# Kernel tuning notes

Measured on AMD Instinct MI355X. Metric: run time of the kernel, lower is better.

## Reference

```python
import jax, jax.numpy as jnp
import numpy as np
from jax import lax

DIM = 384
NUM_HEADS = 6
STRIDE_Q = 1
STRIDE_KV = 2
BN_EPS = 1e-5
SCALE = DIM ** (-0.5)  # CvT scales by dim_out, not head_dim


def setup_inputs() -> dict:
    key = jax.random.key(0)
    ks = jax.random.split(key, 8)
    B, H, W, C = 32, 28, 28, DIM
    T = 1 + H * W
    x = jax.random.normal(ks[0], (B, T, C), dtype=jnp.float32)
    conv_w = jax.random.normal(ks[1], (3, C, 1, 3, 3), dtype=jnp.float32) * 0.1
    bn_gamma = jnp.ones((3, C), dtype=jnp.float32)
    bn_beta = jnp.zeros((3, C), dtype=jnp.float32)
    bn_mean = jnp.zeros((3, C), dtype=jnp.float32)
    bn_var = jnp.ones((3, C), dtype=jnp.float32)
    w_q = jax.random.normal(ks[2], (C, C), dtype=jnp.float32) * 0.02
    w_k = jax.random.normal(ks[3], (C, C), dtype=jnp.float32) * 0.02
    w_v = jax.random.normal(ks[4], (C, C), dtype=jnp.float32) * 0.02
    w_proj = jax.random.normal(ks[5], (C, C), dtype=jnp.float32) * 0.02
    b_proj = jnp.zeros((C,), dtype=jnp.float32)
    return {"x": x, "conv_w": conv_w, "bn_gamma": bn_gamma, "bn_beta": bn_beta,
            "bn_mean": bn_mean, "bn_var": bn_var, "w_q": w_q, "w_k": w_k,
            "w_v": w_v, "w_proj": w_proj, "b_proj": b_proj, "h": H, "w": W}


def _dw_conv_bn(x_sp, cw, gamma, beta, mean, var, stride):
    # x_sp: [B, C, H, W]; cw: [C, 1, 3, 3] depthwise (groups=C); inference BN
    C = x_sp.shape[1]
    y = lax.conv_general_dilated(
        x_sp, cw, window_strides=(stride, stride), padding=((1, 1), (1, 1)),
        feature_group_count=C, dimension_numbers=("NCHW", "OIHW", "NCHW"))
    inv = gamma * lax.rsqrt(var + BN_EPS)
    y = y * inv[None, :, None, None] + (beta - mean * inv)[None, :, None, None]
    B, Cc, Hc, Wc = y.shape
    return y.reshape(B, Cc, Hc * Wc).transpose(0, 2, 1)  # b (h w) c


def reference(x, conv_w, bn_gamma, bn_beta, bn_mean, bn_var,
              w_q, w_k, w_v, w_proj, b_proj, h, w):
    B, T, C = x.shape
    nh, hd = NUM_HEADS, C // NUM_HEADS
    cls_tok, x_tok = x[:, :1], x[:, 1:]
    x_sp = x_tok.reshape(B, h, w, C).transpose(0, 3, 1, 2)  # b c h w

    q = _dw_conv_bn(x_sp, conv_w[0], bn_gamma[0], bn_beta[0], bn_mean[0], bn_var[0], STRIDE_Q)
    k = _dw_conv_bn(x_sp, conv_w[1], bn_gamma[1], bn_beta[1], bn_mean[1], bn_var[1], STRIDE_KV)
    v = _dw_conv_bn(x_sp, conv_w[2], bn_gamma[2], bn_beta[2], bn_mean[2], bn_var[2], STRIDE_KV)

    q = jnp.concatenate([cls_tok, q], axis=1)
    k = jnp.concatenate([cls_tok, k], axis=1)
    v = jnp.concatenate([cls_tok, v], axis=1)

    def split_heads(t, wm):  # linear proj then b t (h d) -> b h t d
        t = t @ wm.T
        Bt, Tt, _ = t.shape
        return t.reshape(Bt, Tt, nh, hd).transpose(0, 2, 1, 3)

    q = split_heads(q, w_q)
    k = split_heads(k, w_k)
    v = split_heads(v, w_v)

    attn = jax.nn.softmax(jnp.einsum("bhld,bhtd->bhlt", q, k) * SCALE, axis=-1)
    out = jnp.einsum("bhlt,bhtd->bhld", attn, v)
    out = out.transpose(0, 2, 1, 3).reshape(B, -1, C)  # b t (h d)
    return out @ w_proj.T + b_proj
```

## Files before the change

kernel.cpp:

```cpp
#include <hip/hip_runtime.h>
#include <math.h>

#define B_SZ   32
#define C_DIM  384
#define H_IN   28
#define W_IN   28
#define TQ     785
#define TKV    197
#define NH     6
#define HD     64
#define SCALE_F 0.05103103630798287f
#define SCALE_L2E (0.05103103630798287f * 1.4426950408889634f)
#define BN_EPS_F 1e-5f

#define QROWS    25120
#define KVROWS   6304
#define QROWS_P  25344
#define KVROWS_P 6400
#define WELEM    147456
#define VT_LD    208

#define QT256    99
#define KVT256   25

typedef _Float16 f16;
typedef f16  f16x8 __attribute__((ext_vector_type(8)));
typedef f16  f16x4 __attribute__((ext_vector_type(4)));
typedef float f32x4 __attribute__((ext_vector_type(4)));

__device__ __forceinline__ void split16(float v, f16& h, f16& l) {
    h = (f16)v;
    l = (f16)(v - (float)h);
}

__device__ __forceinline__ void cp16(void* lds, const void* g) {
    __builtin_amdgcn_global_load_lds(
        (const __attribute__((address_space(1))) unsigned int*)g,
        (__attribute__((address_space(3))) unsigned int*)lds, 16, 0, 0);
}

__device__ __forceinline__ bool swz(int id, int yMax, int& y, int& n0) {
    int g = id / 24, w = id - g * 24;
    y = g * 8 + (w & 7);
    n0 = (w >> 3) * 128;
    return y < yMax;
}

__global__ __launch_bounds__(256) void prep_kernel(
    const float* __restrict__ wq, const float* __restrict__ wk,
    const float* __restrict__ wv, const float* __restrict__ wp,
    const float* __restrict__ conv_w,
    const float* __restrict__ gamma, const float* __restrict__ beta,
    const float* __restrict__ mean, const float* __restrict__ var,
    f16* __restrict__ Wh, f16* __restrict__ Wl,
    float* __restrict__ wAll)
{
    int idx = blockIdx.x * 256 + threadIdx.x;
    if (idx < 4 * WELEM) {
        int which = idx / WELEM, rem = idx - which * WELEM;
        const float* s = (which == 0) ? wq : (which == 1) ? wk : (which == 2) ? wv : wp;
        float v = s[rem];
        if (which == 0) v *= SCALE_L2E;
        f16 h, l;
        split16(v, h, l);
        Wh[idx] = h; Wl[idx] = l;
    } else if (idx < 4 * WELEM + 3 * C_DIM) {
        int k = idx - 4 * WELEM;
        int cv = k / C_DIM, c = k - cv * C_DIM;
        float inv = gamma[k] * rsqrtf(var[k] + BN_EPS_F);
#pragma unroll
        for (int t = 0; t < 9; ++t)
            wAll[cv * 3840 + t * C_DIM + c] = conv_w[(size_t)cv * C_DIM * 9 + c * 9 + t] * inv;
        wAll[cv * 3840 + 9 * C_DIM + c] = beta[k] - mean[k] * inv;
    }
}

__global__ __launch_bounds__(256) void fused_conv_kernel(
    const float* __restrict__ x,
    const float* __restrict__ wAll,
    f16* __restrict__ qh, f16* __restrict__ ql,
    f16* __restrict__ kh, f16* __restrict__ kl,
    f16* __restrict__ vh, f16* __restrict__ vl)
{
    __shared__ float sW[3 * 3840];
    int tid = threadIdx.x;
    int oi = blockIdx.x, b = blockIdx.y;

    if (oi == H_IN) {
        if (tid < 96) {
            int c = tid * 4;
            float4 v = *(const float4*)&x[(size_t)b * TQ * C_DIM + c];
            float a[4] = {v.x, v.y, v.z, v.w};
            f16x4 hv, lv;
#pragma unroll
            for (int u = 0; u < 4; ++u) { f16 h, l; split16(a[u], h, l); hv[u] = h; lv[u] = l; }
            size_t oq = (size_t)b * TQ * C_DIM + c;
            size_t okv = (size_t)b * TKV * C_DIM + c;
            *(f16x4*)&qh[oq] = hv;  *(f16x4*)&ql[oq] = lv;
            *(f16x4*)&kh[okv] = hv; *(f16x4*)&kl[okv] = lv;
            *(f16x4*)&vh[okv] = hv; *(f16x4*)&vl[okv] = lv;
        }
        return;
    }

#pragma unroll
    for (int i = 0; i < 12; ++i) {
        int idx = tid + 256 * i;
        if (idx < 2880) cp16(&sW[idx * 4], &wAll[idx * 4]);
    }
    __syncthreads();

    const size_t xb = (size_t)b * TQ * C_DIM + C_DIM;
    bool oi_even = (oi & 1) == 0;

    for (int it = 0; it < 11; ++it) {
        int idx = tid + 256 * it;
        if (idx >= 28 * 96) break;
        int oj = idx / 96, cg = idx - oj * 96;
        int c = cg * 4;

        float4 xv[9];
#pragma unroll
        for (int di = 0; di < 3; ++di) {
            int ii = oi + di - 1;
            bool rok = (ii >= 0) && (ii < H_IN);
#pragma unroll
            for (int dj = 0; dj < 3; ++dj) {
                int jj = oj + dj - 1;
                bool ok = rok && (jj >= 0) && (jj < W_IN);
                xv[di * 3 + dj] = ok ? *(const float4*)&x[xb + ((size_t)ii * W_IN + jj) * C_DIM + c]
                                     : make_float4(0.f, 0.f, 0.f, 0.f);
            }
        }

        {
            float4 acc = *(const float4*)&sW[0 * 3840 + 9 * C_DIM + c];
#pragma unroll
            for (int t = 0; t < 9; ++t) {
                float4 w4 = *(const float4*)&sW[0 * 3840 + t * C_DIM + c];
                acc.x += w4.x * xv[t].x; acc.y += w4.y * xv[t].y;
                acc.z += w4.z * xv[t].z; acc.w += w4.w * xv[t].w;
            }
            f16x4 hv, lv;
            float a[4] = {acc.x, acc.y, acc.z, acc.w};
#pragma unroll
            for (int u = 0; u < 4; ++u) { f16 h, l; split16(a[u], h, l); hv[u] = h; lv[u] = l; }
            size_t off = ((size_t)b * TQ + 1 + oi * W_IN + oj) * C_DIM + c;
            *(f16x4*)&qh[off] = hv;
            *(f16x4*)&ql[off] = lv;
        }

        if (oi_even && ((oj & 1) == 0)) {
            int p = (oi >> 1) * 14 + (oj >> 1);
            size_t off = ((size_t)b * TKV + 1 + p) * C_DIM + c;
#pragma unroll
            for (int cv = 1; cv <= 2; ++cv) {
                float4 acc = *(const float4*)&sW[cv * 3840 + 9 * C_DIM + c];
#pragma unroll
                for (int t = 0; t < 9; ++t) {
                    float4 w4 = *(const float4*)&sW[cv * 3840 + t * C_DIM + c];
                    acc.x += w4.x * xv[t].x; acc.y += w4.y * xv[t].y;
                    acc.z += w4.z * xv[t].z; acc.w += w4.w * xv[t].w;
                }
                f16x4 hv, lv;
                float a[4] = {acc.x, acc.y, acc.z, acc.w};
#pragma unroll
                for (int u = 0; u < 4; ++u) { f16 h, l; split16(a[u], h, l); hv[u] = h; lv[u] = l; }
                if (cv == 1) { *(f16x4*)&kh[off] = hv; *(f16x4*)&kl[off] = lv; }
                else         { *(f16x4*)&vh[off] = hv; *(f16x4*)&vl[off] = lv; }
            }
        }
    }
}

__device__ __forceinline__ void gemm_body(
    const f16* __restrict__ Ah, const f16* __restrict__ Al,
    const f16* __restrict__ Wh, const f16* __restrict__ Wl,
    const float* __restrict__ bias,
    float* __restrict__ Cf, f16* __restrict__ Coh, f16* __restrict__ Col,
    int M, int mode, int m0, int n0)
{
    __shared__ f16 lds[3 * 24576];

    const int t = threadIdx.x;
    const int wv = t >> 6, lane = t & 63;
    const int wr = (wv >> 1) * 64;
    const int wc = (wv & 1) * 64;
    const int lrow = lane & 15, quad = lane >> 4;
    const int qsw = quad ^ ((lrow >> 1) & 3);

    const int sr = t >> 2;
    const int g  = (t & 3) ^ ((t >> 3) & 3);

    const f16* gA0h = Ah + (size_t)(m0 + sr) * 384 + g * 8;
    const f16* gA1h = gA0h + 128 * 384;
    const f16* gA0l = Al + (size_t)(m0 + sr) * 384 + g * 8;
    const f16* gA1l = gA0l + 128 * 384;
    const f16* gBh  = Wh + (size_t)(n0 + sr) * 384 + g * 8;
    const f16* gBl  = Wl + (size_t)(n0 + sr) * 384 + g * 8;

#define STAGE(buf, kk) do {                                   \
        f16* d = lds + (buf) * 24576 + t * 8;                 \
        const int ko = (kk) * 32;                             \
        cp16(d,         gA0h + ko);                           \
        cp16(d + 4096,  gA1h + ko);                           \
        cp16(d + 8192,  gA0l + ko);                           \
        cp16(d + 12288, gA1l + ko);                           \
        cp16(d + 16384, gBh + ko);                            \
        cp16(d + 20480, gBl + ko);                            \
    } while (0)

    f32x4 acc[4][4];
#pragma unroll
    for (int i = 0; i < 4; ++i)
#pragma unroll
        for (int j = 0; j < 4; ++j)
            acc[i][j] = (f32x4){0.f, 0.f, 0.f, 0.f};

    STAGE(0, 0);
    STAGE(1, 1);

#pragma unroll
    for (int kk = 0; kk < 12; ++kk) {
        if (kk == 11) asm volatile("s_waitcnt vmcnt(0)" ::: "memory");
        else          asm volatile("s_waitcnt vmcnt(6)" ::: "memory");
        __builtin_amdgcn_s_barrier();
        __builtin_amdgcn_sched_barrier(0);

        if (kk < 10) {
            STAGE((kk + 2) % 3, kk + 2);
            __builtin_amdgcn_sched_barrier(0);
        }

        const f16* bp = lds + (kk % 3) * 24576;
        f16x8 ah[4], al[4], bh[4], bl[4];
#pragma unroll
        for (int i = 0; i < 4; ++i) {
            int ro = (wr + i * 16 + lrow) * 32 + qsw * 8;
            ah[i] = *(const f16x8*)&bp[ro];
            al[i] = *(const f16x8*)&bp[8192 + ro];
        }
#pragma unroll
        for (int j = 0; j < 4; ++j) {
            int ro = (wc + j * 16 + lrow) * 32 + qsw * 8;
            bh[j] = *(const f16x8*)&bp[16384 + ro];
            bl[j] = *(const f16x8*)&bp[20480 + ro];
        }
        asm volatile("s_waitcnt lgkmcnt(0)" ::: "memory");
        __builtin_amdgcn_sched_barrier(0);

        __builtin_amdgcn_s_setprio(1);
#pragma unroll
        for (int i = 0; i < 4; ++i)
#pragma unroll
            for (int j = 0; j < 4; ++j) {
                acc[i][j] = __builtin_amdgcn_mfma_f32_16x16x32_f16(ah[i], bh[j], acc[i][j], 0, 0, 0);
                acc[i][j] = __builtin_amdgcn_mfma_f32_16x16x32_f16(ah[i], bl[j], acc[i][j], 0, 0, 0);
                acc[i][j] = __builtin_amdgcn_mfma_f32_16x16x32_f16(al[i], bh[j], acc[i][j], 0, 0, 0);
            }
        __builtin_amdgcn_s_setprio(0);
    }
#undef STAGE

#pragma unroll
    for (int i = 0; i < 4; ++i) {
        int grow0 = m0 + wr + i * 16 + quad * 4;
#pragma unroll
        for (int j = 0; j < 4; ++j) {
            int gcol = n0 + wc + j * 16 + lrow;
            float bb = (bias && mode == 0) ? bias[gcol] : 0.f;
#pragma unroll
            for (int r = 0; r < 4; ++r) {
                int grow = grow0 + r;
                if (grow >= M) continue;
                float v = acc[i][j][r] + bb;
                if (mode == 0) {
                    Cf[(size_t)grow * 384 + gcol] = v;
                } else if (mode == 1) {
                    f16 h, l;
                    split16(v, h, l);
                    Coh[(size_t)grow * 384 + gcol] = h;
                    Col[(size_t)grow * 384 + gcol] = l;
                } else {
                    int bb2 = grow / TKV;
                    int key = grow - bb2 * TKV;
                    size_t off = (size_t)bb2 * 384 * VT_LD + (size_t)gcol * VT_LD + key;
                    f16 h, l;
                    split16(v, h, l);
                    Coh[off] = h;
                    Col[off] = l;
                }
            }
        }
    }
}

__global__ __launch_bounds__(512, 2) void qkv_proj_kernel(
    const f16* __restrict__ qh, const f16* __restrict__ ql,
    const f16* __restrict__ kh, const f16* __restrict__ kl,
    const f16* __restrict__ vh, const f16* __restrict__ vl,
    const f16* __restrict__ Wh, const f16* __restrict__ Wl,
    f16* __restrict__ Qph, f16* __restrict__ Qpl,
    f16* __restrict__ Kph, f16* __restrict__ Kpl,
    f16* __restrict__ VTh, f16* __restrict__ VTl,
    int yMax)
{
    int y, n0;
    if (!swz(blockIdx.x, yMax, y, n0)) return;
    if (y < QT256)
        gemm_body(qh, ql, Wh, Wl, nullptr, nullptr, Qph, Qpl, QROWS, 1, y * 256, n0);
    else if (y < QT256 + KVT256)
        gemm_body(kh, kl, Wh + WELEM, Wl + WELEM, nullptr, nullptr, Kph, Kpl,
                  KVROWS, 1, (y - QT256) * 256, n0);
    else
        gemm_body(vh, vl, Wh + 2 * WELEM, Wl + 2 * WELEM, nullptr, nullptr, VTh, VTl,
                  KVROWS, 2, (y - QT256 - KVT256) * 256, n0);
}

__global__ __launch_bounds__(512, 2) void v_proj_kernel(
    const f16* __restrict__ vh, const f16* __restrict__ vl,
    const f16* __restrict__ Wh, const f16* __restrict__ Wl,
    f16* __restrict__ VTh, f16* __restrict__ VTl)
{
    int y, n0;
    if (!swz(blockIdx.x, KVT256, y, n0)) return;
    gemm_body(vh, vl, Wh, Wl, nullptr, nullptr, VTh, VTl, KVROWS, 2, y * 256, n0);
}

__global__ __launch_bounds__(512, 2) void out_proj_kernel(
    const f16* __restrict__ Ah, const f16* __restrict__ Al,
    const f16* __restrict__ Wh, const f16* __restrict__ Wl,
    const float* __restrict__ bias, float* __restrict__ Cf)
{
    int y, n0;
    if (!swz(blockIdx.x, QT256, y, n0)) return;
    gemm_body(Ah, Al, Wh, Wl, bias, Cf, nullptr, nullptr, QROWS, 0, y * 256, n0);
}

__global__ __launch_bounds__(256) void attn_mfma4(
    const f16* __restrict__ Qh, const f16* __restrict__ Ql,
    const f16* __restrict__ Kh, const f16* __restrict__ Kl,
    const f16* __restrict__ VTh, const f16* __restrict__ VTl,
    f16* __restrict__ Oh, f16* __restrict__ Ol)
{
    __shared__ f16 sQh[2][64][32];
    __shared__ f16 sQl[2][64][32];
    __shared__ f16 sKh[2][64][32];
    __shared__ f16 sKl[2][64][32];
    __shared__ float sPs[64][68];

    int t = threadIdx.x;
    int wv = t >> 6, lane = t & 63;
    int c = lane & 15, quad = lane >> 4;
    int wq0 = wv * 16;
    int h = blockIdx.y, b = blockIdx.z;
    int q0 = blockIdx.x * 64;

    const size_t qbase  = (size_t)b * TQ * C_DIM + h * HD;
    const size_t kbase  = (size_t)b * TKV * C_DIM + h * HD;
    const size_t vtbase = (size_t)b * 384 * VT_LD + (size_t)h * HD * VT_LD;

#pragma unroll
    for (int i = 0; i < 2; ++i) {
        int idx = t + 256 * i;
        int ks = idx >> 8, row = (idx >> 2) & 63, sg = (idx & 3) * 8;
        cp16(&sQh[ks][row][sg], &Qh[qbase + (size_t)(q0 + row) * C_DIM + ks * 32 + sg]);
        cp16(&sQl[ks][row][sg], &Ql[qbase + (size_t)(q0 + row) * C_DIM + ks * 32 + sg]);
    }

    f32x4 s[4][4];
#pragma unroll
    for (int kt = 0; kt < 4; ++kt)
#pragma unroll
        for (int j = 0; j < 4; ++j)
            s[kt][j] = (f32x4){0.f, 0.f, 0.f, 0.f};

#pragma unroll
    for (int kt = 0; kt < 4; ++kt) {
        if (kt) __syncthreads();
#pragma unroll
        for (int i = 0; i < 2; ++i) {
            int idx = t + 256 * i;
            int ks = idx >> 8, row = (idx >> 2) & 63, sg = (idx & 3) * 8;
            cp16(&sKh[ks][row][sg], &Kh[kbase + (size_t)(kt * 64 + row) * C_DIM + ks * 32 + sg]);
            cp16(&sKl[ks][row][sg], &Kl[kbase + (size_t)(kt * 64 + row) * C_DIM + ks * 32 + sg]);
        }
        __syncthreads();

#pragma unroll
        for (int ks = 0; ks < 2; ++ks) {
            f16x8 qh8 = *(const f16x8*)&sQh[ks][wq0 + c][quad * 8];
            f16x8 ql8 = *(const f16x8*)&sQl[ks][wq0 + c][quad * 8];
#pragma unroll
            for (int j = 0; j < 4; ++j) {
                f16x8 kh8 = *(const f16x8*)&sKh[ks][j * 16 + c][quad * 8];
                f16x8 kl8 = *(const f16x8*)&sKl[ks][j * 16 + c][quad * 8];
                s[kt][j] = __builtin_amdgcn_mfma_f32_16x16x32_f16(qh8, kh8, s[kt][j], 0, 0, 0);
                s[kt][j] = __builtin_amdgcn_mfma_f32_16x16x32_f16(qh8, kl8, s[kt][j], 0, 0, 0);
                s[kt][j] = __builtin_amdgcn_mfma_f32_16x16x32_f16(ql8, kh8, s[kt][j], 0, 0, 0);
            }
        }
    }

    __syncthreads();

#pragma unroll
    for (int i = 0; i < 2; ++i) {
        int idx = t + 256 * i;
        int ks = idx >> 8, row = (idx >> 2) & 63, sg = (idx & 3) * 8;
        cp16(&sKh[ks][row][sg], &VTh[vtbase + (size_t)row * VT_LD + ks * 32 + sg]);
        cp16(&sKl[ks][row][sg], &VTl[vtbase + (size_t)row * VT_LD + ks * 32 + sg]);
    }

#pragma unroll
    for (int r = 0; r < 4; ++r) {
        s[3][0][r] = (c < 5) ? s[3][0][r] : -1e30f;
        s[3][1][r] = -1e30f;
        s[3][2][r] = -1e30f;
        s[3][3][r] = -1e30f;
    }

    float inv_r[4];
#pragma unroll
    for (int r = 0; r < 4; ++r) {
        float mx = -1e30f;
#pragma unroll
        for (int kt = 0; kt < 4; ++kt)
#pragma unroll
            for (int j = 0; j < 4; ++j)
                mx = fmaxf(mx, s[kt][j][r]);
        mx = fmaxf(mx, __shfl_xor(mx, 1));
        mx = fmaxf(mx, __shfl_xor(mx, 2));
        mx = fmaxf(mx, __shfl_xor(mx, 4));
        mx = fmaxf(mx, __shfl_xor(mx, 8));
        float sum = 0.f;
#pragma unroll
        for (int kt = 0; kt < 4; ++kt)
#pragma unroll
            for (int j = 0; j < 4; ++j) {
                float pv = exp2f(s[kt][j][r] - mx);
                s[kt][j][r] = pv;
                sum += pv;
            }
        sum += __shfl_xor(sum, 1);
        sum += __shfl_xor(sum, 2);
        sum += __shfl_xor(sum, 4);
        sum += __shfl_xor(sum, 8);
        inv_r[r] = 1.f / sum;
    }

    f32x4 o[4];
#pragma unroll
    for (int j = 0; j < 4; ++j) o[j] = (f32x4){0.f, 0.f, 0.f, 0.f};

#pragma unroll
    for (int vt = 0; vt < 4; ++vt) {
#pragma unroll
        for (int r = 0; r < 4; ++r)
#pragma unroll
            for (int j = 0; j < 4; ++j)
                sPs[wq0 + quad * 4 + r][j * 16 + c] = s[vt][j][r];

        __syncthreads();

#pragma unroll
        for (int ks = 0; ks < 2; ++ks) {
            float4 p0 = *(const float4*)&sPs[wq0 + c][ks * 32 + quad * 8];
            float4 p1 = *(const float4*)&sPs[wq0 + c][ks * 32 + quad * 8 + 4];
            float pf[8] = {p0.x, p0.y, p0.z, p0.w, p1.x, p1.y, p1.z, p1.w};
            f16x8 ph8, pl8;
#pragma unroll
            for (int ii = 0; ii < 8; ++ii) {
                f16 hh, ll;
                split16(pf[ii], hh, ll);
                ph8[ii] = hh; pl8[ii] = ll;
            }
#pragma unroll
            for (int j = 0; j < 4; ++j) {
                f16x8 vh8 = *(const f16x8*)&sKh[ks][j * 16 + c][quad * 8];
                f16x8 vl8 = *(const f16x8*)&sKl[ks][j * 16 + c][quad * 8];
                o[j] = __builtin_amdgcn_mfma_f32_16x16x32_f16(ph8, vh8, o[j], 0, 0, 0);
                o[j] = __builtin_amdgcn_mfma_f32_16x16x32_f16(ph8, vl8, o[j], 0, 0, 0);
                o[j] = __builtin_amdgcn_mfma_f32_16x16x32_f16(pl8, vh8, o[j], 0, 0, 0);
            }
        }

        if (vt < 3) {
            __syncthreads();
#pragma unroll
            for (int i = 0; i < 2; ++i) {
                int idx = t + 256 * i;
                int ks = idx >> 8, row = (idx >> 2) & 63, sg = (idx & 3) * 8;
                cp16(&sKh[ks][row][sg],
                     &VTh[vtbase + (size_t)row * VT_LD + (vt + 1) * 64 + ks * 32 + sg]);
                cp16(&sKl[ks][row][sg],
                     &VTl[vtbase + (size_t)row * VT_LD + (vt + 1) * 64 + ks * 32 + sg]);
            }
        }
    }

#pragma unroll
    for (int r = 0; r < 4; ++r) {
        int gq = q0 + wq0 + quad * 4 + r;
        if (gq >= TQ) continue;
        float inv = inv_r[r];
#pragma unroll
        for (int j = 0; j < 4; ++j) {
            float v = o[j][r] * inv;
            f16 hh, ll;
            split16(v, hh, ll);
            size_t off = (size_t)(b * TQ + gq) * C_DIM + h * HD + j * 16 + c;
            Oh[off] = hh;
            Ol[off] = ll;
        }
    }
}

extern "C" void kernel_launch(void* const* d_in, const int* in_sizes, int n_in,
                              void* d_out, int out_size, void* d_ws, size_t ws_size,
                              hipStream_t stream) {
    const float* x       = (const float*)d_in[0];
    const float* conv_w  = (const float*)d_in[1];
    const float* bn_g    = (const float*)d_in[2];
    const float* bn_b    = (const float*)d_in[3];
    const float* bn_m    = (const float*)d_in[4];
    const float* bn_v    = (const float*)d_in[5];
    const float* w_q     = (const float*)d_in[6];
    const float* w_k     = (const float*)d_in[7];
    const float* w_v     = (const float*)d_in[8];
    const float* w_proj  = (const float*)d_in[9];
    const float* b_proj  = (const float*)d_in[10];
    float* out = (float*)d_out;

    const size_t QSZ   = (size_t)QROWS_P * 384 * sizeof(f16);
    const size_t KVSZ  = (size_t)KVROWS_P * 384 * sizeof(f16);
    const size_t WSZ   = 4 * (size_t)WELEM * sizeof(f16);
    const size_t VTSZ  = (size_t)B_SZ * 384 * VT_LD * sizeof(f16);
    const size_t WALLS = 3 * 3840 * sizeof(float);

    char* p = (char*)d_ws;
    f16* qh  = (f16*)p; p += QSZ;
    f16* ql  = (f16*)p; p += QSZ;
    f16* vh  = (f16*)p; p += KVSZ;
    f16* vl  = (f16*)p; p += KVSZ;
    f16* kh  = (f16*)p; p += KVSZ;
    f16* kl  = (f16*)p; p += KVSZ;
    f16* Wh  = (f16*)p; p += WSZ;
    f16* Wl  = (f16*)p; p += WSZ;
    f16* Qph = (f16*)p; p += QSZ;
    f16* Qpl = (f16*)p; p += QSZ;
    f16* Kph = (f16*)p; p += KVSZ;
    f16* Kpl = (f16*)p; p += KVSZ;
    float* wAll = (float*)p; p += WALLS;

    size_t used = (size_t)(p - (char*)d_ws);
    bool sepVT = (ws_size >= used + 2 * VTSZ);
    f16 *VTh, *VTl;
    if (sepVT) {
        VTh = (f16*)p;
        VTl = VTh + (size_t)B_SZ * 384 * VT_LD;
    } else {
        VTh = kh;
        VTl = VTh + (size_t)B_SZ * 384 * VT_LD;
    }
    f16* oh = qh;
    f16* ol = ql;

    {
        int total = 4 * WELEM + 3 * C_DIM;
        prep_kernel<<<(total + 255) / 256, 256, 0, stream>>>(
            w_q, w_k, w_v, w_proj, conv_w, bn_g, bn_b, bn_m, bn_v, Wh, Wl, wAll);
    }

    {
        dim3 gc(H_IN + 1, B_SZ);
        fused_conv_kernel<<<gc, 256, 0, stream>>>(x, wAll, qh, ql, kh, kl, vh, vl);
    }

    if (sepVT) {
        int yMax = QT256 + 2 * KVT256;
        int nb = ((yMax + 7) / 8) * 24;
        qkv_proj_kernel<<<nb, 512, 0, stream>>>(qh, ql, kh, kl, vh, vl, Wh, Wl,
                                                Qph, Qpl, Kph, Kpl, VTh, VTl, yMax);
    } else {
        int yMax = QT256 + KVT256;
        int nb = ((yMax + 7) / 8) * 24;
        qkv_proj_kernel<<<nb, 512, 0, stream>>>(qh, ql, kh, kl, vh, vl, Wh, Wl,
                                                Qph, Qpl, Kph, Kpl, VTh, VTl, yMax);
        int nbv = ((KVT256 + 7) / 8) * 24;
        v_proj_kernel<<<nbv, 512, 0, stream>>>(vh, vl, Wh + 2 * WELEM, Wl + 2 * WELEM,
                                               VTh, VTl);
    }

    {
        dim3 ga((TQ + 63) / 64, NH, B_SZ);
        attn_mfma4<<<ga, 256, 0, stream>>>(Qph, Qpl, Kph, Kpl, VTh, VTl, oh, ol);
    }

    {
        int nb = ((QT256 + 7) / 8) * 24;
        out_proj_kernel<<<nb, 512, 0, stream>>>(oh, ol, Wh + 3 * WELEM, Wl + 3 * WELEM,
                                                b_proj, out);
    }
}
```

Before: 303.3 us.

## Drop low-half split for V, attention probs and attention output

Stores V^T, the softmax probabilities and the attention output as single fp16 instead of hi/lo split pairs. This cuts the PV MFMAs from three per tile to one and removes the Vl/Ol buffers. The output projection gets a new lighter GEMM body that loads only the A high part, uses a three-stage LDS pipeline and issues two MFMAs per tile. The V tile prefetch is rescheduled into double buffers across the four key tiles. In exchange, accuracy for V, P and O drops to plain fp16.

After: 271.6 us. 1.12x faster.

```diff
diff --git a/kernel.cpp b/kernel.cpp
--- a/kernel.cpp
+++ b/kernel.cpp
@@ -16,7 +16,7 @@
 #define QROWS    25120
 #define KVROWS   6304
 #define QROWS_P  25344
-#define KVROWS_P 6400
+#define KVROWS_P 6528
 #define WELEM    147456
 #define VT_LD    208
 
@@ -285,11 +285,107 @@
                     int bb2 = grow / TKV;
                     int key = grow - bb2 * TKV;
                     size_t off = (size_t)bb2 * 384 * VT_LD + (size_t)gcol * VT_LD + key;
-                    f16 h, l;
-                    split16(v, h, l);
-                    Coh[off] = h;
-                    Col[off] = l;
+                    Coh[off] = (f16)v;
                 }
+            }
+        }
+    }
+}
+
+__device__ __forceinline__ void gemm_body_s(
+    const f16* __restrict__ Ah,
+    const f16* __restrict__ Wh, const f16* __restrict__ Wl,
+    const float* __restrict__ bias, float* __restrict__ Cf,
+    int M, int m0, int n0)
+{
+    __shared__ f16 lds[3 * 16384];
+
+    const int t = threadIdx.x;
+    const int wv = t >> 6, lane = t & 63;
+    const int wr = (wv >> 1) * 64;
+    const int wc = (wv & 1) * 64;
+    const int lrow = lane & 15, quad = lane >> 4;
+    const int qsw = quad ^ ((lrow >> 1) & 3);
+
+    const int sr = t >> 2;
+    const int g  = (t & 3) ^ ((t >> 3) & 3);
+
+    const f16* gA0 = Ah + (size_t)(m0 + sr) * 384 + g * 8;
+    const f16* gA1 = gA0 + 128 * 384;
+    const f16* gBh = Wh + (size_t)(n0 + sr) * 384 + g * 8;
+    const f16* gBl = Wl + (size_t)(n0 + sr) * 384 + g * 8;
+
+#define STAGE_S(buf, kk) do {                                 \
+        f16* d = lds + (buf) * 16384 + t * 8;                 \
+        const int ko = (kk) * 32;                             \
+        cp16(d,         gA0 + ko);                            \
+        cp16(d + 4096,  gA1 + ko);                            \
+        cp16(d + 8192,  gBh + ko);                            \
+        cp16(d + 12288, gBl + ko);                            \
+    } while (0)
+
+    f32x4 acc[4][4];
+#pragma unroll
+    for (int i = 0; i < 4; ++i)
+#pragma unroll
+        for (int j = 0; j < 4; ++j)
+            acc[i][j] = (f32x4){0.f, 0.f, 0.f, 0.f};
+
+    STAGE_S(0, 0);
+    STAGE_S(1, 1);
+
+#pragma unroll
+    for (int kk = 0; kk < 12; ++kk) {
+        if (kk == 11) asm volatile("s_waitcnt vmcnt(0)" ::: "memory");
+        else          asm volatile("s_waitcnt vmcnt(4)" ::: "memory");
+        __builtin_amdgcn_s_barrier();
+        __builtin_amdgcn_sched_barrier(0);
+
+        if (kk < 10) {
+            STAGE_S((kk + 2) % 3, kk + 2);
+            __builtin_amdgcn_sched_barrier(0);
+        }
+
+        const f16* bp = lds + (kk % 3) * 16384;
+        f16x8 ah[4], bh[4], bl[4];
+#pragma unroll
+        for (int i = 0; i < 4; ++i) {
+            int ro = (wr + i * 16 + lrow) * 32 + qsw * 8;
+            ah[i] = *(const f16x8*)&bp[ro];
+        }
+#pragma unroll
+        for (int j = 0; j < 4; ++j) {
+            int ro = (wc + j * 16 + lrow) * 32 + qsw * 8;
+            bh[j] = *(const f16x8*)&bp[8192 + ro];
+            bl[j] = *(const f16x8*)&bp[12288 + ro];
+        }
+        asm volatile("s_waitcnt lgkmcnt(0)" ::: "memory");
+        __builtin_amdgcn_sched_barrier(0);
+
+        __builtin_amdgcn_s_setprio(1);
+#pragma unroll
+        for (int i = 0; i < 4; ++i)
+#pragma unroll
+            for (int j = 0; j < 4; ++j) {
+                acc[i][j] = __builtin_amdgcn_mfma_f32_16x16x32_f16(ah[i], bh[j], acc[i][j], 0, 0, 0);
+                acc[i][j] = __builtin_amdgcn_mfma_f32_16x16x32_f16(ah[i], bl[j], acc[i][j], 0, 0, 0);
+            }
+        __builtin_amdgcn_s_setprio(0);
+    }
+#undef STAGE_S
+
+#pragma unroll
+    for (int i = 0; i < 4; ++i) {
+        int grow0 = m0 + wr + i * 16 + quad * 4;
+#pragma unroll
+        for (int j = 0; j < 4; ++j) {
+            int gcol = n0 + wc + j * 16 + lrow;
+            float bb = bias[gcol];
+#pragma unroll
+            for (int r = 0; r < 4; ++r) {
+                int grow = grow0 + r;
+                if (grow >= M) continue;
+                Cf[(size_t)grow * 384 + gcol] = acc[i][j][r] + bb;
             }
         }
     }
@@ -302,7 +398,7 @@
     const f16* __restrict__ Wh, const f16* __restrict__ Wl,
     f16* __restrict__ Qph, f16* __restrict__ Qpl,
     f16* __restrict__ Kph, f16* __restrict__ Kpl,
-    f16* __restrict__ VTh, f16* __restrict__ VTl,
+    f16* __restrict__ VTh,
     int yMax)
 {
     int y, n0;
@@ -313,35 +409,35 @@
         gemm_body(kh, kl, Wh + WELEM, Wl + WELEM, nullptr, nullptr, Kph, Kpl,
                   KVROWS, 1, (y - QT256) * 256, n0);
     else
-        gemm_body(vh, vl, Wh + 2 * WELEM, Wl + 2 * WELEM, nullptr, nullptr, VTh, VTl,
+        gemm_body(vh, vl, Wh + 2 * WELEM, Wl + 2 * WELEM, nullptr, nullptr, VTh, nullptr,
                   KVROWS, 2, (y - QT256 - KVT256) * 256, n0);
 }
 
 __global__ __launch_bounds__(512, 2) void v_proj_kernel(
     const f16* __restrict__ vh, const f16* __restrict__ vl,
     const f16* __restrict__ Wh, const f16* __restrict__ Wl,
-    f16* __restrict__ VTh, f16* __restrict__ VTl)
+    f16* __restrict__ VTh)
 {
     int y, n0;
     if (!swz(blockIdx.x, KVT256, y, n0)) return;
-    gemm_body(vh, vl, Wh, Wl, nullptr, nullptr, VTh, VTl, KVROWS, 2, y * 256, n0);
+    gemm_body(vh, vl, Wh, Wl, nullptr, nullptr, VTh, nullptr, KVROWS, 2, y * 256, n0);
 }
 
 __global__ __launch_bounds__(512, 2) void out_proj_kernel(
-    const f16* __restrict__ Ah, const f16* __restrict__ Al,
+    const f16* __restrict__ Ah,
     const f16* __restrict__ Wh, const f16* __restrict__ Wl,
     const float* __restrict__ bias, float* __restrict__ Cf)
 {
     int y, n0;
     if (!swz(blockIdx.x, QT256, y, n0)) return;
-    gemm_body(Ah, Al, Wh, Wl, bias, Cf, nullptr, nullptr, QROWS, 0, y * 256, n0);
-}
-
-__global__ __launch_bounds__(256) void attn_mfma4(
+    gemm_body_s(Ah, Wh, Wl, bias, Cf, QROWS, y * 256, n0);
+}
+
+__global__ __launch_bounds__(256) void attn_mfma6(
     const f16* __restrict__ Qh, const f16* __restrict__ Ql,
     const f16* __restrict__ Kh, const f16* __restrict__ Kl,
-    const f16* __restrict__ VTh, const f16* __restrict__ VTl,
-    f16* __restrict__ Oh, f16* __restrict__ Ol)
+    const f16* __restrict__ VTh,
+    f16* __restrict__ Oh)
 {
     __shared__ f16 sQh[2][64][32];
     __shared__ f16 sQl[2][64][32];
@@ -409,7 +505,7 @@
         int idx = t + 256 * i;
         int ks = idx >> 8, row = (idx >> 2) & 63, sg = (idx & 3) * 8;
         cp16(&sKh[ks][row][sg], &VTh[vtbase + (size_t)row * VT_LD + ks * 32 + sg]);
-        cp16(&sKl[ks][row][sg], &VTl[vtbase + (size_t)row * VT_LD + ks * 32 + sg]);
+        cp16(&sKl[ks][row][sg], &VTh[vtbase + (size_t)row * VT_LD + 64 + ks * 32 + sg]);
     }
 
 #pragma unroll
@@ -453,51 +549,46 @@
 #pragma unroll
     for (int j = 0; j < 4; ++j) o[j] = (f32x4){0.f, 0.f, 0.f, 0.f};
 
-#pragma unroll
-    for (int vt = 0; vt < 4; ++vt) {
-#pragma unroll
-        for (int r = 0; r < 4; ++r)
-#pragma unroll
-            for (int j = 0; j < 4; ++j)
-                sPs[wq0 + quad * 4 + r][j * 16 + c] = s[vt][j][r];
-
-        __syncthreads();
-
-#pragma unroll
-        for (int ks = 0; ks < 2; ++ks) {
-            float4 p0 = *(const float4*)&sPs[wq0 + c][ks * 32 + quad * 8];
-            float4 p1 = *(const float4*)&sPs[wq0 + c][ks * 32 + quad * 8 + 4];
-            float pf[8] = {p0.x, p0.y, p0.z, p0.w, p1.x, p1.y, p1.z, p1.w};
-            f16x8 ph8, pl8;
-#pragma unroll
-            for (int ii = 0; ii < 8; ++ii) {
-                f16 hh, ll;
-                split16(pf[ii], hh, ll);
-                ph8[ii] = hh; pl8[ii] = ll;
-            }
-#pragma unroll
-            for (int j = 0; j < 4; ++j) {
-                f16x8 vh8 = *(const f16x8*)&sKh[ks][j * 16 + c][quad * 8];
-                f16x8 vl8 = *(const f16x8*)&sKl[ks][j * 16 + c][quad * 8];
-                o[j] = __builtin_amdgcn_mfma_f32_16x16x32_f16(ph8, vh8, o[j], 0, 0, 0);
-                o[j] = __builtin_amdgcn_mfma_f32_16x16x32_f16(ph8, vl8, o[j], 0, 0, 0);
-                o[j] = __builtin_amdgcn_mfma_f32_16x16x32_f16(pl8, vh8, o[j], 0, 0, 0);
-            }
-        }
-
-        if (vt < 3) {
-            __syncthreads();
-#pragma unroll
-            for (int i = 0; i < 2; ++i) {
-                int idx = t + 256 * i;
-                int ks = idx >> 8, row = (idx >> 2) & 63, sg = (idx & 3) * 8;
-                cp16(&sKh[ks][row][sg],
-                     &VTh[vtbase + (size_t)row * VT_LD + (vt + 1) * 64 + ks * 32 + sg]);
-                cp16(&sKl[ks][row][sg],
-                     &VTl[vtbase + (size_t)row * VT_LD + (vt + 1) * 64 + ks * 32 + sg]);
-            }
-        }
-    }
+#define SPS_WRITE(VT) do {                                           \
+        _Pragma("unroll") for (int r = 0; r < 4; ++r)                \
+            _Pragma("unroll") for (int j = 0; j < 4; ++j)            \
+                sPs[wq0 + quad * 4 + r][j * 16 + c] = s[VT][j][r];   \
+    } while (0)
+
+#define VT_ISSUE2(DST, VT) do {                                                \
+        _Pragma("unroll") for (int i = 0; i < 2; ++i) {                        \
+            int idx = t + 256 * i;                                             \
+            int ks = idx >> 8, row = (idx >> 2) & 63, sg = (idx & 3) * 8;      \
+            cp16(&DST[ks][row][sg],                                            \
+                 &VTh[vtbase + (size_t)row * VT_LD + (VT) * 64 + ks * 32 + sg]); \
+        } } while (0)
+
+#define PV_TILE_S(BUF) do {                                                    \
+        _Pragma("unroll") for (int ks = 0; ks < 2; ++ks) {                     \
+            float4 p0 = *(const float4*)&sPs[wq0 + c][ks * 32 + quad * 8];     \
+            float4 p1 = *(const float4*)&sPs[wq0 + c][ks * 32 + quad * 8 + 4]; \
+            float pf[8] = {p0.x, p0.y, p0.z, p0.w, p1.x, p1.y, p1.z, p1.w};    \
+            f16x8 p8;                                                          \
+            _Pragma("unroll") for (int ii = 0; ii < 8; ++ii) p8[ii] = (f16)pf[ii]; \
+            _Pragma("unroll") for (int j = 0; j < 4; ++j) {                    \
+                f16x8 vv8 = *(const f16x8*)&BUF[ks][j * 16 + c][quad * 8];     \
+                o[j] = __builtin_amdgcn_mfma_f32_16x16x32_f16(p8, vv8, o[j], 0, 0, 0); \
+            } } } while (0)
+
+    __syncthreads();
+    SPS_WRITE(0);
+    PV_TILE_S(sKh);
+    __syncthreads();
+    VT_ISSUE2(sKh, 2);
+    SPS_WRITE(1);
+    PV_TILE_S(sKl);
+    __syncthreads();
+    VT_ISSUE2(sKl, 3);
+    SPS_WRITE(2);
+    PV_TILE_S(sKh);
+    __syncthreads();
+    SPS_WRITE(3);
+    PV_TILE_S(sKl);
 
 #pragma unroll
     for (int r = 0; r < 4; ++r) {
@@ -506,14 +597,13 @@
         float inv = inv_r[r];
 #pragma unroll
         for (int j = 0; j < 4; ++j) {
-            float v = o[j][r] * inv;
-            f16 hh, ll;
-            split16(v, hh, ll);
             size_t off = (size_t)(b * TQ + gq) * C_DIM + h * HD + j * 16 + c;
-            Oh[off] = hh;
-            Ol[off] = ll;
-        }
-    }
+            Oh[off] = (f16)(o[j][r] * inv);
+        }
+    }
+#undef SPS_WRITE
+#undef VT_ISSUE2
+#undef PV_TILE_S
 }
 
 extern "C" void kernel_launch(void* const* d_in, const int* in_sizes, int n_in,
@@ -554,17 +644,9 @@
     float* wAll = (float*)p; p += WALLS;
 
     size_t used = (size_t)(p - (char*)d_ws);
-    bool sepVT = (ws_size >= used + 2 * VTSZ);
-    f16 *VTh, *VTl;
-    if (sepVT) {
-        VTh = (f16*)p;
-        VTl = VTh + (size_t)B_SZ * 384 * VT_LD;
-    } else {
-        VTh = kh;
-        VTl = VTh + (size_t)B_SZ * 384 * VT_LD;
-    }
+    bool sepVT = (ws_size >= used + VTSZ);
+    f16* VTh = sepVT ? (f16*)p : kh;
     f16* oh = qh;
-    f16* ol = ql;
 
     {
         int total = 4 * WELEM + 3 * C_DIM;
@@ -581,25 +663,25 @@
         int yMax = QT256 + 2 * KVT256;
         int nb = ((yMax + 7) / 8) * 24;
         qkv_proj_kernel<<<nb, 512, 0, stream>>>(qh, ql, kh, kl, vh, vl, Wh, Wl,
-                                                Qph, Qpl, Kph, Kpl, VTh, VTl, yMax);
+                                                Qph, Qpl, Kph, Kpl, VTh, yMax);
     } else {
         int yMax = QT256 + KVT256;
         int nb = ((yMax + 7) / 8) * 24;
         qkv_proj_kernel<<<nb, 512, 0, stream>>>(qh, ql, kh, kl, vh, vl, Wh, Wl,
-                                                Qph, Qpl, Kph, Kpl, VTh, VTl, yMax);
+                                                Qph, Qpl, Kph, Kpl, VTh, yMax);
         int nbv = ((KVT256 + 7) / 8) * 24;
         v_proj_kernel<<<nbv, 512, 0, stream>>>(vh, vl, Wh + 2 * WELEM, Wl + 2 * WELEM,
-                                               VTh, VTl);
+                                               VTh);
     }
 
     {
         dim3 ga((TQ + 63) / 64, NH, B_SZ);
-        attn_mfma4<<<ga, 256, 0, stream>>>(Qph, Qpl, Kph, Kpl, VTh, VTl, oh, ol);
+        attn_mfma6<<<ga, 256, 0, stream>>>(Qph, Qpl, Kph, Kpl, VTh, oh);
     }
 
     {
         int nb = ((QT256 + 7) / 8) * 24;
-        out_proj_kernel<<<nb, 512, 0, stream>>>(oh, ol, Wh + 3 * WELEM, Wl + 3 * WELEM,
+        out_proj_kernel<<<nb, 512, 0, stream>>>(oh, Wh + 3 * WELEM, Wl + 3 * WELEM,
                                                 b_proj, out);
     }
 }
```
